# Performance work log

Measured on AMD Instinct MI355X. Metric: run time of the kernel, lower is better.

## Reference

```python
import jax, jax.numpy as jnp
import numpy as np

B, S, IN, OUT = 4, 2048, 4096, 16384

def setup_inputs() -> dict:
    key = jax.random.key(0)
    k1, k2, k3, k4 = jax.random.split(key, 4)
    x = jax.random.normal(k1, (B, S, IN), dtype=jnp.float32)
    weight_int = jax.random.randint(k2, (OUT, IN), -128, 128, dtype=jnp.int32)
    # per-row scale, small positive values as produced by quantize_weight
    weight_scale = jax.random.uniform(k3, (OUT, 1), dtype=jnp.float32, minval=1e-3, maxval=2e-2)
    weight_zero_point = jnp.zeros((OUT, 1), dtype=jnp.int32)  # symmetric quantization
    bias = jax.random.normal(k4, (OUT,), dtype=jnp.float32) * 0.02
    return {"x": x, "weight_int": weight_int, "weight_scale": weight_scale,
            "weight_zero_point": weight_zero_point, "bias": bias}

def reference(x, weight_int, weight_scale, weight_zero_point, bias):
    # Dequantize: (int8 - zero_point) * per-row scale -> fp32 weight [OUT, IN]
    weight_fp = (weight_int.astype(jnp.float32) - weight_zero_point.astype(jnp.float32)) * weight_scale
    # F.linear: x @ W^T + b
    out = jnp.einsum('bsi,oi->bso', x, weight_fp) + bias
    return out
```

## Files before the change

### kernel.cpp

```cpp
#include <hip/hip_runtime.h>
#include <hip/hip_bf16.h>

typedef __bf16 bf16x8 __attribute__((ext_vector_type(8)));
typedef float  f32x4  __attribute__((ext_vector_type(4)));
typedef int    i32x4  __attribute__((ext_vector_type(4)));

#define BM 128
#define BN 128
#define BK 128
#define THREADS 256

__device__ __forceinline__ void gload_lds16(const void* g, void* l) {
  __builtin_amdgcn_global_load_lds(
      (const __attribute__((address_space(1))) void*)g,
      (__attribute__((address_space(3))) void*)l, 16, 0, 0);
}

template<int N> __device__ __forceinline__ void vmwait() {
  if constexpr (N == 0)      asm volatile("s_waitcnt vmcnt(0)");
  else if constexpr (N == 8) asm volatile("s_waitcnt vmcnt(8)");
}

__device__ __forceinline__ void tile_barrier() {
  __builtin_amdgcn_sched_barrier(0);
  asm volatile("s_barrier");
  __builtin_amdgcn_sched_barrier(0);
}

__global__ __launch_bounds__(256)
void quant_x(const float* __restrict__ x, signed char* __restrict__ xq,
             float* __restrict__ sx, int* __restrict__ rowsum, int K) {
  const int row = blockIdx.x, tid = threadIdx.x;
  const int wave = tid >> 6, lane = tid & 63;
  const float* xr = x + (long)row * K;
  __shared__ float smax[4];
  __shared__ int   ssum[4];

  float amax = 0.f;
  for (int i = tid * 16; i < K; i += 256 * 16) {
    #pragma unroll
    for (int j = 0; j < 4; ++j) {
      float4 v = *(const float4*)(xr + i + j * 4);
      amax = fmaxf(amax, fmaxf(fmaxf(fabsf(v.x), fabsf(v.y)),
                               fmaxf(fabsf(v.z), fabsf(v.w))));
    }
  }
  #pragma unroll
  for (int m = 32; m >= 1; m >>= 1) amax = fmaxf(amax, __shfl_xor(amax, m));
  if (lane == 0) smax[wave] = amax;
  __syncthreads();
  const float m4 = fmaxf(fmaxf(smax[0], smax[1]), fmaxf(smax[2], smax[3]));
  const float scale = (m4 > 0.f) ? (m4 / 127.f) : 1.f;
  const float inv   = (m4 > 0.f) ? (127.f / m4) : 0.f;

  int lsum = 0;
  for (int i = tid * 16; i < K; i += 256 * 16) {
    union { signed char c[16]; int4 v; } u;
    #pragma unroll
    for (int j = 0; j < 4; ++j) {
      float4 v = *(const float4*)(xr + i + j * 4);
      int q0 = __float2int_rn(v.x * inv), q1 = __float2int_rn(v.y * inv);
      int q2 = __float2int_rn(v.z * inv), q3 = __float2int_rn(v.w * inv);
      u.c[j*4+0] = (signed char)q0; u.c[j*4+1] = (signed char)q1;
      u.c[j*4+2] = (signed char)q2; u.c[j*4+3] = (signed char)q3;
      lsum += q0 + q1 + q2 + q3;
    }
    *(int4*)(xq + (long)row * K + i) = u.v;
  }
  #pragma unroll
  for (int m = 32; m >= 1; m >>= 1) lsum += __shfl_xor(lsum, m);
  if (lane == 0) ssum[wave] = lsum;
  __syncthreads();
  if (tid == 0) {
    rowsum[row] = ssum[0] + ssum[1] + ssum[2] + ssum[3];
    sx[row] = scale;
  }
}

__global__ void conv_w(const int* __restrict__ w, const int* __restrict__ zp,
                       signed char* __restrict__ wq, int K, long n) {
  long i0 = ((long)blockIdx.x * blockDim.x + threadIdx.x) * 16;
  long stride = (long)gridDim.x * blockDim.x * 16;
  for (long i = i0; i < n; i += stride) {
    const int z = zp[i / K];
    union { signed char c[16]; int4 v; } u;
    #pragma unroll
    for (int j = 0; j < 4; ++j) {
      int4 a = *(const int4*)(w + i + j * 4);
      int q0 = min(127, max(-128, a.x - z)), q1 = min(127, max(-128, a.y - z));
      int q2 = min(127, max(-128, a.z - z)), q3 = min(127, max(-128, a.w - z));
      u.c[j*4+0] = (signed char)q0; u.c[j*4+1] = (signed char)q1;
      u.c[j*4+2] = (signed char)q2; u.c[j*4+3] = (signed char)q3;
    }
    *(int4*)(wq + i) = u.v;
  }
}

__global__ __launch_bounds__(THREADS, 2)
void qlin_gemm_i8(const signed char* __restrict__ A, const signed char* __restrict__ B,
                  const float* __restrict__ sx, const int* __restrict__ rowsum,
                  const int* __restrict__ zp,
                  const float* __restrict__ scale, const float* __restrict__ bias,
                  float* __restrict__ C, int M, int N, int K) {
  __shared__ alignas(16) signed char As[2][BM * BK];
  __shared__ alignas(16) signed char Bs[2][BN * BK];

  const int tid  = threadIdx.x;
  const int wave = tid >> 6;
  const int lane = tid & 63;
  const int wm = wave >> 1, wn = wave & 1;

  int bid = blockIdx.x, nwg = gridDim.x, swz = bid;
  if ((nwg & 7) == 0) swz = (bid & 7) * (nwg >> 3) + (bid >> 3);
  const int ntn = N / BN;
  const long row0 = (long)(swz / ntn) * BM;
  const long col0 = (long)(swz % ntn) * BN;

  const signed char* Ag = A + row0 * (long)K;
  const signed char* Bg = B + col0 * (long)K;

  const int srow = wave * 8 + (lane >> 3);
  const int kswz = ((lane & 7) ^ (lane >> 3)) * 16;

#define STAGE_A(b, c, kt) gload_lds16(Ag + (long)((c)*32 + srow) * K + (kt) + kswz, \
                                      &As[b][(c)*4096 + wave*1024])
#define STAGE_B(b, c, kt) gload_lds16(Bg + (long)((c)*32 + srow) * K + (kt) + kswz, \
                                      &Bs[b][(c)*4096 + wave*1024])
#define STAGE8(b, kt) { STAGE_B(b,0,kt); STAGE_B(b,1,kt); STAGE_B(b,2,kt); STAGE_B(b,3,kt); \
                        STAGE_A(b,0,kt); STAGE_A(b,1,kt); STAGE_A(b,2,kt); STAGE_A(b,3,kt); }

  const int rsel = lane & 15;
  const int ksl  = lane >> 4;
  const int lan7 = lane & 7;

  i32x4 acc[4][4] = {};
  i32x4 bf[4][2];

#define AF_READ(bb, m, kk)                                                      \
  (*(const i32x4*)&As[bb][(wm*64 + (m)*16 + rsel)*BK                            \
                          + (((((kk)<<2)+ksl) ^ lan7) << 4)])

#define TILE(bb, STAGES, ENDW)                                                   \
  {                                                                              \
    __builtin_amdgcn_s_setprio(1);                                               \
    _Pragma("unroll")                                                            \
    for (int n = 0; n < 4; ++n)                                                  \
      _Pragma("unroll")                                                          \
      for (int kk = 0; kk < 2; ++kk)                                             \
        bf[n][kk] = *(const i32x4*)&Bs[bb][(wn*64 + n*16 + rsel)*BK              \
                                           + ((((kk<<2)+ksl) ^ lan7) << 4)];     \
    i32x4 afp0, afp1;                                                            \
    afp0 = AF_READ(bb, 0, 0);                                                    \
    _Pragma("unroll")                                                            \
    for (int f = 0; f < 8; ++f) {                                                \
      const int m = f & 3, kk = f >> 2;                                          \
      if (f < 7) {                                                               \
        const int m2 = (f + 1) & 3, kk2 = (f + 1) >> 2;                          \
        if (f & 1) afp0 = AF_READ(bb, m2, kk2);                                  \
        else       afp1 = AF_READ(bb, m2, kk2);                                  \
      }                                                                          \
      _Pragma("unroll")                                                          \
      for (int n = 0; n < 4; ++n)                                                \
        acc[m][n] = __builtin_amdgcn_mfma_i32_16x16x64_i8(                       \
            (f & 1) ? afp1 : afp0, bf[n][kk], acc[m][n], 0, 0, 0);               \
    }                                                                            \
    __builtin_amdgcn_s_setprio(0);                                               \
    tile_barrier();                                                     \
    STAGES;                                                                      \
    ENDW;                                                                        \
    tile_barrier();                                                    \
  }

  const int NT = K / BK;

  STAGE8(0, 0)
  STAGE8(1, BK)
  vmwait<8>();
  tile_barrier();

  for (int t = 0; t < NT - 3; t += 2) {
    const long kt2 = (long)(t + 2) * BK;
    const long kt3 = (long)(t + 3) * BK;
    TILE(0, STAGE8(0, kt2), vmwait<8>())
    TILE(1, STAGE8(1, kt3), vmwait<8>())
  }
  TILE(0, (void)0, vmwait<0>())
  TILE(1, (void)0, (void)0)
#undef TILE
#undef AF_READ
#undef STAGE8
#undef STAGE_A
#undef STAGE_B

  float swv[4], bvv[4]; int zpv[4];
  #pragma unroll
  for (int n = 0; n < 4; ++n) {
    const long gcol = col0 + wn * 64 + n * 16 + rsel;
    swv[n] = scale[gcol];
    bvv[n] = bias[gcol];
    zpv[n] = zp[gcol];
  }
  #pragma unroll
  for (int m = 0; m < 4; ++m) {
    const long growb = row0 + wm * 64 + m * 16 + ksl * 4;
    #pragma unroll
    for (int j = 0; j < 4; ++j) {
      const long grow = growb + j;
      const float sxv = sx[grow];
      const int   rsv = rowsum[grow];
      float* orow = C + grow * (long)N;
      #pragma unroll
      for (int n = 0; n < 4; ++n) {
        const long gcol = col0 + wn * 64 + n * 16 + rsel;
        orow[gcol] = (float)(acc[m][n][j] - zpv[n] * rsv) * (sxv * swv[n]) + bvv[n];
      }
    }
  }
}

__global__ __launch_bounds__(256)
void qlin_gemm_small(const float* __restrict__ Af, const int* __restrict__ Bi,
                     const int* __restrict__ zp,
                     const float* __restrict__ scale, const float* __restrict__ bias,
                     float* __restrict__ C, int M, int N, int K) {
  __shared__ alignas(16) __bf16 As[128 * 64];
  __shared__ alignas(16) __bf16 Bs[128 * 64];
  const int tid = threadIdx.x, wave = tid >> 6, lane = tid & 63;
  int bid = blockIdx.x, nwg = gridDim.x, swz = bid;
  if ((nwg & 7) == 0) swz = (bid & 7) * (nwg >> 3) + (bid >> 3);
  const int ntn = N / 128;
  const long row0 = (long)(swz / ntn) * 128, col0 = (long)(swz % ntn) * 128;
  const int wr = wave >> 1, wc = wave & 1;
  f32x4 acc[4][4] = {};
  for (int kt = 0; kt < K; kt += 64) {
    #pragma unroll
    for (int i = 0; i < 4; ++i) {
      const int flat = i * 2048 + tid * 8;
      const int r = flat >> 6, cc = flat & 63;
      const int wcc = ((cc >> 3) ^ (r & 7)) << 3;
      const float* g = Af + (row0 + r) * (long)K + kt + cc;
      float4 f0 = *(const float4*)g; float4 f1 = *(const float4*)(g + 4);
      bf16x8 v;
      v[0]=(__bf16)f0.x; v[1]=(__bf16)f0.y; v[2]=(__bf16)f0.z; v[3]=(__bf16)f0.w;
      v[4]=(__bf16)f1.x; v[5]=(__bf16)f1.y; v[6]=(__bf16)f1.z; v[7]=(__bf16)f1.w;
      *(bf16x8*)(As + r * 64 + wcc) = v;
    }
    #pragma unroll
    for (int i = 0; i < 4; ++i) {
      const int flat = i * 2048 + tid * 8;
      const int r = flat >> 6, cc = flat & 63;
      const int wcc = ((cc >> 3) ^ (r & 7)) << 3;
      const long grow = col0 + r;
      const int z = zp[grow];
      const int* g = Bi + grow * (long)K + kt + cc;
      int4 a = *(const int4*)g; int4 b = *(const int4*)(g + 4);
      bf16x8 v;
      v[0]=(__bf16)(float)(a.x-z); v[1]=(__bf16)(float)(a.y-z);
      v[2]=(__bf16)(float)(a.z-z); v[3]=(__bf16)(float)(a.w-z);
      v[4]=(__bf16)(float)(b.x-z); v[5]=(__bf16)(float)(b.y-z);
      v[6]=(__bf16)(float)(b.z-z); v[7]=(__bf16)(float)(b.w-z);
      *(bf16x8*)(Bs + r * 64 + wcc) = v;
    }
    __syncthreads();
    #pragma unroll
    for (int kk = 0; kk < 2; ++kk) {
      bf16x8 af[4], bfr[4];
      const int rs = lane & 15, ks = kk * 4 + (lane >> 4);
      const int rd = (ks ^ (lane & 7)) << 3;
      #pragma unroll
      for (int m = 0; m < 4; ++m) af[m] = *(const bf16x8*)(As + (wr*64 + m*16 + rs)*64 + rd);
      #pragma unroll
      for (int n = 0; n < 4; ++n) bfr[n] = *(const bf16x8*)(Bs + (wc*64 + n*16 + rs)*64 + rd);
      #pragma unroll
      for (int m = 0; m < 4; ++m)
        #pragma unroll
        for (int n = 0; n < 4; ++n)
          acc[m][n] = __builtin_amdgcn_mfma_f32_16x16x32_bf16(af[m], bfr[n], acc[m][n], 0, 0, 0);
    }
    __syncthreads();
  }
  #pragma unroll
  for (int m = 0; m < 4; ++m) {
    const long grow = row0 + wr * 64 + m * 16 + ((lane >> 4) << 2);
    #pragma unroll
    for (int n = 0; n < 4; ++n) {
      const long gcol = col0 + wc * 64 + n * 16 + (lane & 15);
      const float s = scale[gcol], bb2 = bias[gcol];
      float* o = C + grow * (long)N + gcol;
      #pragma unroll
      for (int j = 0; j < 4; ++j) o[(long)j * N] = acc[m][n][j] * s + bb2;
    }
  }
}

extern "C" void kernel_launch(void* const* d_in, const int* in_sizes, int n_in,
                              void* d_out, int out_size, void* d_ws, size_t ws_size,
                              hipStream_t stream) {
  const float* x    = (const float*)d_in[0];
  const int*   wint = (const int*)d_in[1];
  const float* wsc  = (const float*)d_in[2];
  const int*   wzp  = (const int*)d_in[3];
  const float* bias = (const float*)d_in[4];
  float* out = (float*)d_out;

  const int N = in_sizes[4];
  const int K = in_sizes[1] / N;
  const int M = in_sizes[0] / K;

  const size_t xqb = (size_t)M * K;
  const size_t wqb = (size_t)N * K;
  const size_t sxb = (size_t)M * sizeof(float);
  const size_t rsb = (size_t)M * sizeof(int);
  const int NT = K / BK;

  if (ws_size >= xqb + wqb + sxb + rsb && (M % BM) == 0 && (N % BN) == 0 &&
      (K % BK) == 0 && (K % 4096) == 0 && NT >= 6 && (NT % 2) == 0) {
    signed char* xq = (signed char*)d_ws;
    signed char* wq = xq + xqb;
    float* sx  = (float*)(wq + wqb);
    int* rsum  = (int*)((char*)sx + sxb);
    quant_x<<<M, 256, 0, stream>>>(x, xq, sx, rsum, K);
    conv_w<<<2048, 256, 0, stream>>>(wint, wzp, wq, K, (long)N * K);
    const int grid = (M / BM) * (N / BN);
    qlin_gemm_i8<<<grid, THREADS, 0, stream>>>(xq, wq, sx, rsum, wzp, wsc, bias,
                                               out, M, N, K);
  } else {
    const int grid = (M / 128) * (N / 128);
    qlin_gemm_small<<<grid, 256, 0, stream>>>(x, wint, wzp, wsc, bias, out, M, N, K);
  }
}
```

Measured before the change: 848.7 us.

## Replace double-buffered LDS pipeline with single buffer and raise occupancy to three blocks

Removes the two-stage LDS double buffering in the int8 GEMM, so each K tile is loaded, fully waited on and then computed from a single 32KB buffer. Launch bounds go from 2 to 3 blocks per CU, relying on extra resident workgroups to hide global-load latency in place of the software prefetch. The cost is that loads within a block no longer overlap its MFMA work, and register pressure is tighter under the new occupancy target. The host guard is relaxed because an even tile count is no longer required.

```diff
diff --git a/kernel.cpp b/kernel.cpp
--- a/kernel.cpp
+++ b/kernel.cpp
@@ -16,10 +16,7 @@
       (__attribute__((address_space(3))) void*)l, 16, 0, 0);
 }
 
-template<int N> __device__ __forceinline__ void vmwait() {
-  if constexpr (N == 0)      asm volatile("s_waitcnt vmcnt(0)");
-  else if constexpr (N == 8) asm volatile("s_waitcnt vmcnt(8)");
-}
+__device__ __forceinline__ void vmwait0() { asm volatile("s_waitcnt vmcnt(0)"); }
 
 __device__ __forceinline__ void tile_barrier() {
   __builtin_amdgcn_sched_barrier(0);
@@ -96,14 +93,14 @@
   }
 }
 
-__global__ __launch_bounds__(THREADS, 2)
+__global__ __launch_bounds__(THREADS, 3)
 void qlin_gemm_i8(const signed char* __restrict__ A, const signed char* __restrict__ B,
                   const float* __restrict__ sx, const int* __restrict__ rowsum,
                   const int* __restrict__ zp,
                   const float* __restrict__ scale, const float* __restrict__ bias,
                   float* __restrict__ C, int M, int N, int K) {
-  __shared__ alignas(16) signed char As[2][BM * BK];
-  __shared__ alignas(16) signed char Bs[2][BN * BK];
+  __shared__ alignas(16) signed char As[BM * BK];
+  __shared__ alignas(16) signed char Bs[BN * BK];
 
   const int tid  = threadIdx.x;
   const int wave = tid >> 6;
@@ -122,12 +119,12 @@
   const int srow = wave * 8 + (lane >> 3);
   const int kswz = ((lane & 7) ^ (lane >> 3)) * 16;
 
-#define STAGE_A(b, c, kt) gload_lds16(Ag + (long)((c)*32 + srow) * K + (kt) + kswz, \
-                                      &As[b][(c)*4096 + wave*1024])
-#define STAGE_B(b, c, kt) gload_lds16(Bg + (long)((c)*32 + srow) * K + (kt) + kswz, \
-                                      &Bs[b][(c)*4096 + wave*1024])
-#define STAGE8(b, kt) { STAGE_B(b,0,kt); STAGE_B(b,1,kt); STAGE_B(b,2,kt); STAGE_B(b,3,kt); \
-                        STAGE_A(b,0,kt); STAGE_A(b,1,kt); STAGE_A(b,2,kt); STAGE_A(b,3,kt); }
+#define STAGE_A(c, kt) gload_lds16(Ag + (long)((c)*32 + srow) * K + (kt) + kswz, \
+                                   &As[(c)*4096 + wave*1024])
+#define STAGE_B(c, kt) gload_lds16(Bg + (long)((c)*32 + srow) * K + (kt) + kswz, \
+                                   &Bs[(c)*4096 + wave*1024])
+#define STAGE8(kt) { STAGE_B(0,kt); STAGE_B(1,kt); STAGE_B(2,kt); STAGE_B(3,kt); \
+                     STAGE_A(0,kt); STAGE_A(1,kt); STAGE_A(2,kt); STAGE_A(3,kt); }
 
   const int rsel = lane & 15;
   const int ksl  = lane >> 4;
@@ -136,57 +133,43 @@
   i32x4 acc[4][4] = {};
   i32x4 bf[4][2];
 
-#define AF_READ(bb, m, kk)                                                      \
-  (*(const i32x4*)&As[bb][(wm*64 + (m)*16 + rsel)*BK                            \
-                          + (((((kk)<<2)+ksl) ^ lan7) << 4)])
-
-#define TILE(bb, STAGES, ENDW)                                                   \
-  {                                                                              \
-    __builtin_amdgcn_s_setprio(1);                                               \
-    _Pragma("unroll")                                                            \
-    for (int n = 0; n < 4; ++n)                                                  \
-      _Pragma("unroll")                                                          \
-      for (int kk = 0; kk < 2; ++kk)                                             \
-        bf[n][kk] = *(const i32x4*)&Bs[bb][(wn*64 + n*16 + rsel)*BK              \
-                                           + ((((kk<<2)+ksl) ^ lan7) << 4)];     \
-    i32x4 afp0, afp1;                                                            \
-    afp0 = AF_READ(bb, 0, 0);                                                    \
-    _Pragma("unroll")                                                            \
-    for (int f = 0; f < 8; ++f) {                                                \
-      const int m = f & 3, kk = f >> 2;                                          \
-      if (f < 7) {                                                               \
-        const int m2 = (f + 1) & 3, kk2 = (f + 1) >> 2;                          \
-        if (f & 1) afp0 = AF_READ(bb, m2, kk2);                                  \
-        else       afp1 = AF_READ(bb, m2, kk2);                                  \
-      }                                                                          \
-      _Pragma("unroll")                                                          \
-      for (int n = 0; n < 4; ++n)                                                \
-        acc[m][n] = __builtin_amdgcn_mfma_i32_16x16x64_i8(                       \
-            (f & 1) ? afp1 : afp0, bf[n][kk], acc[m][n], 0, 0, 0);               \
-    }                                                                            \
-    __builtin_amdgcn_s_setprio(0);                                               \
-    tile_barrier();                                                     \
-    STAGES;                                                                      \
-    ENDW;                                                                        \
-    tile_barrier();                                                    \
-  }
+#define AF_READ(m, kk)                                                          \
+  (*(const i32x4*)&As[(wm*64 + (m)*16 + rsel)*BK                                \
+                      + (((((kk)<<2)+ksl) ^ lan7) << 4)])
 
   const int NT = K / BK;
 
-  STAGE8(0, 0)
-  STAGE8(1, BK)
-  vmwait<8>();
-  tile_barrier();
-
-  for (int t = 0; t < NT - 3; t += 2) {
-    const long kt2 = (long)(t + 2) * BK;
-    const long kt3 = (long)(t + 3) * BK;
-    TILE(0, STAGE8(0, kt2), vmwait<8>())
-    TILE(1, STAGE8(1, kt3), vmwait<8>())
-  }
-  TILE(0, (void)0, vmwait<0>())
-  TILE(1, (void)0, (void)0)
-#undef TILE
+  for (int t = 0; t < NT; ++t) {
+    const long kt = (long)t * BK;
+    STAGE8(kt)
+    vmwait0();
+    tile_barrier();
+
+    __builtin_amdgcn_s_setprio(1);
+    #pragma unroll
+    for (int n = 0; n < 4; ++n)
+      #pragma unroll
+      for (int kk = 0; kk < 2; ++kk)
+        bf[n][kk] = *(const i32x4*)&Bs[(wn*64 + n*16 + rsel)*BK
+                                       + ((((kk<<2)+ksl) ^ lan7) << 4)];
+    i32x4 afp0, afp1;
+    afp0 = AF_READ(0, 0);
+    #pragma unroll
+    for (int f = 0; f < 8; ++f) {
+      const int m = f & 3, kk = f >> 2;
+      if (f < 7) {
+        const int m2 = (f + 1) & 3, kk2 = (f + 1) >> 2;
+        if (f & 1) afp0 = AF_READ(m2, kk2);
+        else       afp1 = AF_READ(m2, kk2);
+      }
+      #pragma unroll
+      for (int n = 0; n < 4; ++n)
+        acc[m][n] = __builtin_amdgcn_mfma_i32_16x16x64_i8(
+            (f & 1) ? afp1 : afp0, bf[n][kk], acc[m][n], 0, 0, 0);
+    }
+    __builtin_amdgcn_s_setprio(0);
+    tile_barrier();
+  }
 #undef AF_READ
 #undef STAGE8
 #undef STAGE_A
@@ -314,7 +297,7 @@
   const int NT = K / BK;
 
   if (ws_size >= xqb + wqb + sxb + rsb && (M % BM) == 0 && (N % BN) == 0 &&
-      (K % BK) == 0 && (K % 4096) == 0 && NT >= 6 && (NT % 2) == 0) {
+      (K % BK) == 0 && (K % 4096) == 0 && NT >= 2) {
     signed char* xq = (signed char*)d_ws;
     signed char* wq = xq + xqb;
     float* sx  = (float*)(wq + wqb);
```

After: 789.4 us. -7.0%, faster.
